# Kernel tuning notes

Measured on AMD Instinct MI355X. Metric: run time of the kernel, lower is better.

The kernel has to match this reference:

```python
import jax, jax.numpy as jnp
import numpy as np

DIST_THRESH = 2.0
YAW_THRESH = np.pi / 3
PI = np.pi


def setup_inputs() -> dict:
    key = jax.random.key(0)
    k1, k2, k3 = jax.random.split(key, 3)
    B, K, T = 32, 16, 30
    N, n = 128, 20
    preds = jax.random.normal(k1, (B, K, T, 2), dtype=jnp.float32)
    centerline_nodes = jax.random.normal(k2, (B, N, n, 2), dtype=jnp.float32)
    centerline_node_masks = jax.random.randint(k3, (B, N, n), 0, 2, dtype=jnp.int32)
    return {
        "preds": preds,
        "centerline_nodes": centerline_nodes,
        "centerline_node_masks": centerline_node_masks,
    }


def _yaw_from_traj(traj):
    # traj: (..., L, 2) -> yaw (..., L), first element zero
    dv = traj[..., 1:, :] - traj[..., :-1, :]
    yaw = -jnp.arctan2(dv[..., 0], dv[..., 1])
    zeros = jnp.zeros(yaw.shape[:-1] + (1,), dtype=yaw.dtype)
    return jnp.concatenate([zeros, yaw], axis=-1)


def reference(preds, centerline_nodes, centerline_node_masks):
    B, K, T, _ = preds.shape
    pred_yaw = _yaw_from_traj(preds)                  # (B, K, T)
    node_yaw = _yaw_from_traj(centerline_nodes)       # (B, N, n)

    cn = centerline_nodes.reshape(B, -1, 2)           # (B, Nn, 2)
    mask = centerline_node_masks.reshape(B, -1)       # (B, Nn)
    pts = preds.reshape(B, -1, 2)                     # (B, KT, 2)

    # pairwise euclidean distance via ||a||^2 + ||b||^2 - 2 a.b
    a2 = jnp.sum(cn * cn, axis=-1)                    # (B, Nn)
    b2 = jnp.sum(pts * pts, axis=-1)                  # (B, KT)
    d2 = a2[:, :, None] + b2[:, None, :] - 2.0 * jnp.einsum("bnd,bkd->bnk", cn, pts)
    dists = jnp.sqrt(jnp.maximum(d2, 0.0))            # (B, Nn, KT)
    dists = jnp.where((mask == 1)[:, :, None], jnp.inf, dists)

    yaw_diffs = node_yaw.reshape(B, -1)[:, :, None] - pred_yaw.reshape(B, -1)[:, None, :]
    yaw_diffs = (yaw_diffs + PI) % (2.0 * PI) - PI    # wrap to [-pi, pi)

    cost = jax.nn.relu(dists - DIST_THRESH) + jax.nn.relu(jnp.abs(yaw_diffs) - YAW_THRESH)
    consistency = jnp.min(cost, axis=1)               # (B, KT)
    return consistency.reshape(B, K, T).sum(axis=-1)  # (B, K)
```

## Files before the change

kernel.cpp:

```cpp
#include <hip/hip_runtime.h>
#include <math.h>

#define B_     32
#define K_     16
#define T_     30
#define KT_    480
#define N_     128
#define NPN_   20
#define NODES_ 2560
#define CH_    32
#define CSZ_   80

#define PI_F      3.14159265358979323846f
#define TWO_PI_F  6.28318530717958647692f
#define YAW_TH_F  (PI_F / 3.0f)

#define NNODE_TOT (B_ * NODES_)
#define NPT_TOT   (B_ * KT_)

#define WS_PTS_OFF   NNODE_TOT
#define WS_PART_OFF4 (NNODE_TOT + NPT_TOT)

__global__ __launch_bounds__(256) void cm_prep(
    const float* __restrict__ preds,
    const float* __restrict__ cn,
    const int*   __restrict__ cmask,
    float4*      __restrict__ ws)
{
  const int idx = blockIdx.x * 256 + threadIdx.x;
  if (idx < NNODE_TOT) {
    const int b  = idx / NODES_;
    const int g  = idx - b * NODES_;
    const int j  = g % NPN_;
    const float2* cnb = (const float2*)cn + (size_t)b * NODES_;
    const float2 p = cnb[g];
    float yaw = 0.0f;
    if (j != 0) {
      const float2 q = cnb[g - 1];
      yaw = -atan2f(p.x - q.x, p.y - q.y);
    }
    const int mv = cmask[idx];
    const float a2 = (mv == 1) ? INFINITY : fmaf(p.x, p.x, p.y * p.y);
    ws[idx] = make_float4(-2.0f * p.x, -2.0f * p.y, a2, yaw);
  } else {
    const int i2 = idx - NNODE_TOT;
    const int b  = i2 / KT_;
    const int kt = i2 - b * KT_;
    const float2* pb = (const float2*)preds + (size_t)b * KT_;
    const float2 pp = pb[kt];
    float pyaw = 0.0f;
    if ((kt % T_) != 0) {
      const float2 pq = pb[kt - 1];
      pyaw = -atan2f(pp.x - pq.x, pp.y - pq.y);
    }
    const float b2 = fmaf(pp.x, pp.x, pp.y * pp.y);
    ws[WS_PTS_OFF + i2] = make_float4(pp.x, pp.y, b2, pyaw);
  }
}

__global__ __launch_bounds__(256) void cm_main(
    const float4* __restrict__ ws_nodes,
    const float4* __restrict__ ws_pts,
    float*        __restrict__ ws_part)
{
  const int b   = blockIdx.x >> 5;
  const int c   = blockIdx.x & (CH_ - 1);
  const int tid = threadIdx.x;

  __shared__ float4 nd[CSZ_];
  if (tid < CSZ_) {
    nd[tid] = ws_nodes[(size_t)b * NODES_ + c * CSZ_ + tid];
  }

  const int kt0 = tid;
  const int kt1 = tid + 256;
  const float4 p0 = ws_pts[(size_t)b * KT_ + kt0];
  const float4 p1 = (kt1 < KT_) ? ws_pts[(size_t)b * KT_ + kt1]
                                : make_float4(0.f, 0.f, 0.f, 0.f);
  __syncthreads();

  float m0 = INFINITY, m1 = INFINITY;
  #pragma unroll 8
  for (int i = 0; i < CSZ_; ++i) {
    const float4 nv = nd[i];
    {
      float t = nv.z + p0.z;
      t = fmaf(nv.x, p0.x, t);
      t = fmaf(nv.y, p0.y, t);
      t = fmaxf(t, 4.0f);
      const float s  = __builtin_amdgcn_sqrtf(t);
      const float yd = nv.w - p0.w;
      const float w2 = TWO_PI_F - fabsf(yd);
      const float a  = fminf(fabsf(yd), w2);
      const float yc = fmaxf(a - YAW_TH_F, 0.0f);
      m0 = fminf(m0, s + yc);
    }
    {
      float t = nv.z + p1.z;
      t = fmaf(nv.x, p1.x, t);
      t = fmaf(nv.y, p1.y, t);
      t = fmaxf(t, 4.0f);
      const float s  = __builtin_amdgcn_sqrtf(t);
      const float yd = nv.w - p1.w;
      const float w2 = TWO_PI_F - fabsf(yd);
      const float a  = fminf(fabsf(yd), w2);
      const float yc = fmaxf(a - YAW_TH_F, 0.0f);
      m1 = fminf(m1, s + yc);
    }
  }

  float* wp = ws_part + ((size_t)b * CH_ + c) * KT_;
  wp[kt0] = m0;
  if (kt1 < KT_) wp[kt1] = m1;
}

__global__ __launch_bounds__(512) void cm_reduce(
    const float* __restrict__ ws_part, float* __restrict__ out)
{
  const int b   = blockIdx.x;
  const int tid = threadIdx.x;
  __shared__ float sc[KT_];

  if (tid < KT_) {
    const float* wp = ws_part + (size_t)b * CH_ * KT_;
    float m = INFINITY;
    #pragma unroll
    for (int c = 0; c < CH_; ++c) m = fminf(m, wp[c * KT_ + tid]);
    sc[tid] = m - 2.0f;
  }
  __syncthreads();

  if (tid < K_) {
    float s = 0.0f;
    #pragma unroll
    for (int t = 0; t < T_; ++t) s += sc[tid * T_ + t];
    out[b * K_ + tid] = s;
  }
}

extern "C" void kernel_launch(void* const* d_in, const int* in_sizes, int n_in,
                              void* d_out, int out_size, void* d_ws, size_t ws_size,
                              hipStream_t stream) {
  const float* preds = (const float*)d_in[0];
  const float* cn    = (const float*)d_in[1];
  const int*   cmask = (const int*)d_in[2];
  float* out = (float*)d_out;
  float4* ws4 = (float4*)d_ws;
  float*  ws_part = (float*)(ws4 + WS_PART_OFF4);

  cm_prep<<<dim3((NNODE_TOT + NPT_TOT) / 256), dim3(256), 0, stream>>>(
      preds, cn, cmask, ws4);
  cm_main<<<dim3(B_ * CH_), dim3(256), 0, stream>>>(
      ws4, ws4 + WS_PTS_OFF, ws_part);
  cm_reduce<<<dim3(B_), dim3(512), 0, stream>>>(ws_part, out);
}
```

Baseline: 75.99 us.

## Fuse prep, main and reduce kernels with a last-block atomic reduction

Node and point preprocessing (yaw via atan2, squared norms, mask) moves into the main kernel, so each block computes its own node chunk and point features instead of reading them from a workspace written by a separate kernel. The final min-over-chunks and sum run in whichever block per batch finishes last, detected with an atomic counter, which removes the separate reduce kernel. A tiny init kernel zeroes the counters, so there are two launches instead of three. In exchange, point yaw atan2 work is repeated by every one of the 32 chunk blocks per batch, and the atomics add fence overhead.

```diff
diff --git a/kernel.cpp b/kernel.cpp
--- a/kernel.cpp
+++ b/kernel.cpp
@@ -15,68 +15,68 @@
 #define TWO_PI_F  6.28318530717958647692f
 #define YAW_TH_F  (PI_F / 3.0f)
 
-#define NNODE_TOT (B_ * NODES_)
-#define NPT_TOT   (B_ * KT_)
+#define WS_PART_ELEMS (B_ * CH_ * KT_)
 
-#define WS_PTS_OFF   NNODE_TOT
-#define WS_PART_OFF4 (NNODE_TOT + NPT_TOT)
+__global__ __launch_bounds__(64) void cm_init(unsigned int* __restrict__ ctr) {
+  if (threadIdx.x < B_) ctr[threadIdx.x] = 0u;
+}
 
-__global__ __launch_bounds__(256) void cm_prep(
+__global__ __launch_bounds__(256) void cm_fused(
     const float* __restrict__ preds,
     const float* __restrict__ cn,
     const int*   __restrict__ cmask,
-    float4*      __restrict__ ws)
-{
-  const int idx = blockIdx.x * 256 + threadIdx.x;
-  if (idx < NNODE_TOT) {
-    const int b  = idx / NODES_;
-    const int g  = idx - b * NODES_;
-    const int j  = g % NPN_;
-    const float2* cnb = (const float2*)cn + (size_t)b * NODES_;
-    const float2 p = cnb[g];
-    float yaw = 0.0f;
-    if (j != 0) {
-      const float2 q = cnb[g - 1];
-      yaw = -atan2f(p.x - q.x, p.y - q.y);
-    }
-    const int mv = cmask[idx];
-    const float a2 = (mv == 1) ? INFINITY : fmaf(p.x, p.x, p.y * p.y);
-    ws[idx] = make_float4(-2.0f * p.x, -2.0f * p.y, a2, yaw);
-  } else {
-    const int i2 = idx - NNODE_TOT;
-    const int b  = i2 / KT_;
-    const int kt = i2 - b * KT_;
-    const float2* pb = (const float2*)preds + (size_t)b * KT_;
-    const float2 pp = pb[kt];
-    float pyaw = 0.0f;
-    if ((kt % T_) != 0) {
-      const float2 pq = pb[kt - 1];
-      pyaw = -atan2f(pp.x - pq.x, pp.y - pq.y);
-    }
-    const float b2 = fmaf(pp.x, pp.x, pp.y * pp.y);
-    ws[WS_PTS_OFF + i2] = make_float4(pp.x, pp.y, b2, pyaw);
-  }
-}
-
-__global__ __launch_bounds__(256) void cm_main(
-    const float4* __restrict__ ws_nodes,
-    const float4* __restrict__ ws_pts,
-    float*        __restrict__ ws_part)
+    float*        __restrict__ ws_part,
+    unsigned int* __restrict__ ctr,
+    float*        __restrict__ out)
 {
   const int b   = blockIdx.x >> 5;
   const int c   = blockIdx.x & (CH_ - 1);
   const int tid = threadIdx.x;
 
   __shared__ float4 nd[CSZ_];
+  __shared__ int    s_last;
+  __shared__ float  sc[KT_];
+
   if (tid < CSZ_) {
-    nd[tid] = ws_nodes[(size_t)b * NODES_ + c * CSZ_ + tid];
+    const int gn = c * CSZ_ + tid;
+    const int j  = gn % NPN_;
+    const float2* cnb = (const float2*)cn + (size_t)b * NODES_;
+    const float2 p = cnb[gn];
+    float yaw = 0.0f;
+    if (j != 0) {
+      const float2 q = cnb[gn - 1];
+      yaw = -atan2f(p.x - q.x, p.y - q.y);
+    }
+    const int mv = cmask[(size_t)b * NODES_ + gn];
+    const float a2 = (mv == 1) ? INFINITY : fmaf(p.x, p.x, p.y * p.y);
+    nd[tid] = make_float4(-2.0f * p.x, -2.0f * p.y, a2, yaw);
   }
 
   const int kt0 = tid;
   const int kt1 = tid + 256;
-  const float4 p0 = ws_pts[(size_t)b * KT_ + kt0];
-  const float4 p1 = (kt1 < KT_) ? ws_pts[(size_t)b * KT_ + kt1]
-                                : make_float4(0.f, 0.f, 0.f, 0.f);
+  const float2* pb = (const float2*)preds + (size_t)b * KT_;
+  float4 p0, p1;
+  {
+    const float2 pp = pb[kt0];
+    float pyaw = 0.0f;
+    if ((kt0 % T_) != 0) {
+      const float2 pq = pb[kt0 - 1];
+      pyaw = -atan2f(pp.x - pq.x, pp.y - pq.y);
+    }
+    p0 = make_float4(pp.x, pp.y, fmaf(pp.x, pp.x, pp.y * pp.y), pyaw);
+  }
+  if (kt1 < KT_) {
+    const float2 pp = pb[kt1];
+    float pyaw = 0.0f;
+    if ((kt1 % T_) != 0) {
+      const float2 pq = pb[kt1 - 1];
+      pyaw = -atan2f(pp.x - pq.x, pp.y - pq.y);
+    }
+    p1 = make_float4(pp.x, pp.y, fmaf(pp.x, pp.x, pp.y * pp.y), pyaw);
+  } else {
+    p1 = make_float4(0.f, 0.f, 0.f, 0.f);
+  }
+
   __syncthreads();
 
   float m0 = INFINITY, m1 = INFINITY;
@@ -90,8 +90,7 @@
       t = fmaxf(t, 4.0f);
       const float s  = __builtin_amdgcn_sqrtf(t);
       const float yd = nv.w - p0.w;
-      const float w2 = TWO_PI_F - fabsf(yd);
-      const float a  = fminf(fabsf(yd), w2);
+      const float a  = fminf(fabsf(yd), TWO_PI_F - fabsf(yd));
       const float yc = fmaxf(a - YAW_TH_F, 0.0f);
       m0 = fminf(m0, s + yc);
     }
@@ -102,8 +101,7 @@
       t = fmaxf(t, 4.0f);
       const float s  = __builtin_amdgcn_sqrtf(t);
       const float yd = nv.w - p1.w;
-      const float w2 = TWO_PI_F - fabsf(yd);
-      const float a  = fminf(fabsf(yd), w2);
+      const float a  = fminf(fabsf(yd), TWO_PI_F - fabsf(yd));
       const float yc = fmaxf(a - YAW_TH_F, 0.0f);
       m1 = fminf(m1, s + yc);
     }
@@ -112,24 +110,31 @@
   float* wp = ws_part + ((size_t)b * CH_ + c) * KT_;
   wp[kt0] = m0;
   if (kt1 < KT_) wp[kt1] = m1;
-}
 
-__global__ __launch_bounds__(512) void cm_reduce(
-    const float* __restrict__ ws_part, float* __restrict__ out)
-{
-  const int b   = blockIdx.x;
-  const int tid = threadIdx.x;
-  __shared__ float sc[KT_];
+  __syncthreads();
+  if (tid == 0) {
+    __threadfence();
+    const unsigned int prev = __hip_atomic_fetch_add(
+        &ctr[b], 1u, __ATOMIC_ACQ_REL, __HIP_MEMORY_SCOPE_AGENT);
+    s_last = (prev == CH_ - 1) ? 1 : 0;
+  }
+  __syncthreads();
+  if (!s_last) return;
 
-  if (tid < KT_) {
-    const float* wp = ws_part + (size_t)b * CH_ * KT_;
+  __threadfence();
+  for (int kt = tid; kt < KT_; kt += 256) {
+    const float* col = ws_part + (size_t)b * CH_ * KT_ + kt;
     float m = INFINITY;
     #pragma unroll
-    for (int c = 0; c < CH_; ++c) m = fminf(m, wp[c * KT_ + tid]);
-    sc[tid] = m - 2.0f;
+    for (int cc = 0; cc < CH_; ++cc) {
+      const float v = __hip_atomic_load(col + cc * KT_,
+                                        __ATOMIC_RELAXED,
+                                        __HIP_MEMORY_SCOPE_AGENT);
+      m = fminf(m, v);
+    }
+    sc[kt] = m - 2.0f;
   }
   __syncthreads();
-
   if (tid < K_) {
     float s = 0.0f;
     #pragma unroll
@@ -145,12 +150,10 @@
   const float* cn    = (const float*)d_in[1];
   const int*   cmask = (const int*)d_in[2];
   float* out = (float*)d_out;
-  float4* ws4 = (float4*)d_ws;
-  float*  ws_part = (float*)(ws4 + WS_PART_OFF4);
+  float* ws_part = (float*)d_ws;
+  unsigned int* ctr = (unsigned int*)(ws_part + WS_PART_ELEMS);
 
-  cm_prep<<<dim3((NNODE_TOT + NPT_TOT) / 256), dim3(256), 0, stream>>>(
-      preds, cn, cmask, ws4);
-  cm_main<<<dim3(B_ * CH_), dim3(256), 0, stream>>>(
-      ws4, ws4 + WS_PTS_OFF, ws_part);
-  cm_reduce<<<dim3(B_), dim3(512), 0, stream>>>(ws_part, out);
+  cm_init<<<dim3(1), dim3(64), 0, stream>>>(ctr);
+  cm_fused<<<dim3(B_ * CH_), dim3(256), 0, stream>>>(
+      preds, cn, cmask, ws_part, ctr, out);
 }
```

Result: slower. 115.6 us (+52.1%).
